# Performance work log

Measured on AMD Instinct MI355X. Metric: run time of the kernel, lower is better.

Reference implementation:

```python
import jax, jax.numpy as jnp
import numpy as np

B, K, N, D = 64, 16, 65536, 256


def setup_inputs() -> dict:
    key = jax.random.key(0)
    ks = jax.random.split(key, 7)
    slots = jax.random.normal(ks[0], (B, K, D), dtype=jnp.float32)
    attention_maps = jax.random.uniform(ks[1], (B, K, N), dtype=jnp.float32)
    semantic_confidence = jax.random.uniform(ks[2], (B, K), dtype=jnp.float32)
    # quality_net params: Linear(D, D//4) -> ReLU -> Dropout(eval: identity) -> Linear(D//4, 1) -> Sigmoid
    H = D // 4
    W1 = jax.random.normal(ks[3], (D, H), dtype=jnp.float32) / np.sqrt(D)
    b1 = jnp.zeros((H,), dtype=jnp.float32)
    W2 = jax.random.normal(ks[4], (H, 1), dtype=jnp.float32) / np.sqrt(H)
    b2 = jnp.zeros((1,), dtype=jnp.float32)
    return {"slots": slots, "attention_maps": attention_maps,
            "semantic_confidence": semantic_confidence,
            "W1": W1, "b1": b1, "W2": W2, "b2": b2}


def reference(slots, attention_maps, semantic_confidence, W1, b1, W2, b2):
    Bk, Kk, Nk = attention_maps.shape
    winners = jnp.argmax(attention_maps, axis=1)                      # [B, N]
    # one-hot winner mask [B, K, N] (replaces the Python K-loop in the source)
    mask = (winners[:, None, :] == jnp.arange(Kk)[None, :, None]).astype(attention_maps.dtype)
    winning_attn = jnp.sum(attention_maps * mask, axis=2)             # [B, K]
    total_attn = jnp.sum(attention_maps, axis=2)                      # [B, K]
    attn_quality = winning_attn / (total_attn + 1e-8)

    # learned quality: tiny MLP (dropout is identity at eval)
    h = jax.nn.relu(jnp.einsum('bkd,dh->bkh', slots, W1) + b1)
    learned_quality = jax.nn.sigmoid(jnp.einsum('bkh,ho->bko', h, W2) + b2)[..., 0]  # [B, K]

    w_attn, w_learned, w_conf = 0.4, 0.4, 0.2
    quality = w_attn * attn_quality + w_learned * learned_quality
    quality = quality * w_conf + semantic_confidence * (1.0 - w_conf)
    return quality
```

## Files before the change

### kernel.cpp

```cpp
#include <hip/hip_runtime.h>
#include <math.h>

#define B_ 64
#define K_ 16
#define N_ 65536
#define D_ 256
#define H_ 64

#define N4_ (N_ / 4)
#define CHUNKS_ 32
#define TPB_ 256
#define COLS_ (N4_ / CHUNKS_)
#define ITERS_ (COLS_ / TPB_)

typedef float f32x4 __attribute__((ext_vector_type(4)));


__global__ __launch_bounds__(TPB_) void attn_stats_kernel(const float* __restrict__ attn,
                                                          float* __restrict__ ws) {
    const int b = blockIdx.x / CHUNKS_;
    const int chunk = blockIdx.x % CHUNKS_;
    const f32x4* base = reinterpret_cast<const f32x4*>(attn) + (size_t)b * K_ * N4_;

    float tot[K_], win[K_];
#pragma unroll
    for (int k = 0; k < K_; ++k) { tot[k] = 0.0f; win[k] = 0.0f; }

#pragma unroll
    for (int it = 0; it < ITERS_; ++it) {
        const int c = chunk * COLS_ + it * TPB_ + threadIdx.x;
        f32x4 f = __builtin_nontemporal_load(&base[c]);
        float m0 = f.x, m1 = f.y, m2 = f.z, m3 = f.w;
        int i0 = 0, i1 = 0, i2 = 0, i3 = 0;
        tot[0] += (f.x + f.y) + (f.z + f.w);
#pragma unroll
        for (int k = 1; k < K_; ++k) {
            f = __builtin_nontemporal_load(&base[(size_t)k * N4_ + c]);
            tot[k] += (f.x + f.y) + (f.z + f.w);
            if (f.x > m0) { m0 = f.x; i0 = k; }
            if (f.y > m1) { m1 = f.y; i1 = k; }
            if (f.z > m2) { m2 = f.z; i2 = k; }
            if (f.w > m3) { m3 = f.w; i3 = k; }
        }
#pragma unroll
        for (int k = 0; k < K_; ++k) {
            win[k] += ((i0 == k) ? m0 : 0.0f) + ((i1 == k) ? m1 : 0.0f) +
                      ((i2 == k) ? m2 : 0.0f) + ((i3 == k) ? m3 : 0.0f);
        }
    }

#pragma unroll
    for (int k = 0; k < K_; ++k) {
        float t = tot[k], w = win[k];
#pragma unroll
        for (int s = 1; s < 64; s <<= 1) {
            t += __shfl_xor(t, s, 64);
            w += __shfl_xor(w, s, 64);
        }
        tot[k] = t; win[k] = w;
    }

    __shared__ float s_tot[4][K_];
    __shared__ float s_win[4][K_];
    const int lane = threadIdx.x & 63;
    const int wv = threadIdx.x >> 6;
    if (lane == 0) {
#pragma unroll
        for (int k = 0; k < K_; ++k) { s_tot[wv][k] = tot[k]; s_win[wv][k] = win[k]; }
    }
    __syncthreads();
    if (threadIdx.x < 2 * K_) {
        const int k = threadIdx.x & (K_ - 1);
        float v;
        if (threadIdx.x < K_) {
            v = (s_tot[0][k] + s_tot[1][k]) + (s_tot[2][k] + s_tot[3][k]);
        } else {
            v = (s_win[0][k] + s_win[1][k]) + (s_win[2][k] + s_win[3][k]);
        }
        ws[(size_t)blockIdx.x * (2 * K_) + threadIdx.x] = v;
    }
}

__global__ __launch_bounds__(64) void finalize_kernel(const float* __restrict__ slots,
                                                      const float* __restrict__ conf,
                                                      const float* __restrict__ W1,
                                                      const float* __restrict__ b1,
                                                      const float* __restrict__ W2,
                                                      const float* __restrict__ b2,
                                                      const float* __restrict__ ws,
                                                      float* __restrict__ out) {
    const int bk = blockIdx.x;
    const int b = bk / K_;
    const int k = bk % K_;
    const int j = threadIdx.x;

    __shared__ float s_slot[D_];
    reinterpret_cast<float4*>(s_slot)[j] =
        reinterpret_cast<const float4*>(slots + (size_t)bk * D_)[j];

    const int ch = j & 31;
    float red = (j < 32) ? ws[(size_t)(b * CHUNKS_ + ch) * (2 * K_) + k]
                         : ws[(size_t)(b * CHUNKS_ + ch) * (2 * K_) + K_ + k];
#pragma unroll
    for (int s = 1; s < 32; s <<= 1) red += __shfl_xor(red, s, 64);

    __syncthreads();

    float acc = b1[j];
#pragma unroll 8
    for (int d = 0; d < D_; ++d) {
        acc = fmaf(s_slot[d], W1[d * H_ + j], acc);
    }
    const float h = fmaxf(acc, 0.0f);
    float val = h * W2[j];
#pragma unroll
    for (int s = 1; s < 64; s <<= 1) val += __shfl_xor(val, s, 64);

    const float w = __shfl(red, 32, 64);
    if (j == 0) {
        const float t = red;
        const float lq = 1.0f / (1.0f + expf(-(val + b2[0])));
        const float aq = w / (t + 1e-8f);
        const float q = 0.4f * aq + 0.4f * lq;
        out[bk] = q * 0.2f + conf[bk] * 0.8f;
    }
}

extern "C" void kernel_launch(void* const* d_in, const int* in_sizes, int n_in,
                              void* d_out, int out_size, void* d_ws, size_t ws_size,
                              hipStream_t stream) {
    const float* slots = (const float*)d_in[0];
    const float* attn  = (const float*)d_in[1];
    const float* conf  = (const float*)d_in[2];
    const float* W1    = (const float*)d_in[3];
    const float* b1    = (const float*)d_in[4];
    const float* W2    = (const float*)d_in[5];
    const float* b2    = (const float*)d_in[6];
    float* out = (float*)d_out;
    float* ws  = (float*)d_ws;

    attn_stats_kernel<<<B_ * CHUNKS_, TPB_, 0, stream>>>(attn, ws);
    finalize_kernel<<<B_ * K_, 64, 0, stream>>>(slots, conf, W1, b1, W2, b2, ws, out);
}
```

Before: 60.96 us.

## Fuse quality MLP into attention stats kernel and use transpose-style wave reduction

Moves the per-slot MLP into the streaming attention-stats kernel. With B*CHUNKS equal to B*K there is one MLP per block, and it runs before or after streaming depending on block parity so its latency can hide behind memory traffic. Halves the chunk count, stops unrolling the outer loop, and replaces the 32 per-register butterfly reductions with a recursive-halving exchange that needs far fewer shuffles. It also writes per-wave partials so the block-level shared-memory reduction goes away. The finalize step becomes a light combine kernel, at the cost of fewer blocks (1024) and extra synchronization inside the streaming kernel.

```diff
diff --git a/kernel.cpp b/kernel.cpp
--- a/kernel.cpp
+++ b/kernel.cpp
@@ -8,27 +8,94 @@
 #define H_ 64
 
 #define N4_ (N_ / 4)
-#define CHUNKS_ 32
+#define CHUNKS_ 16
 #define TPB_ 256
 #define COLS_ (N4_ / CHUNKS_)
 #define ITERS_ (COLS_ / TPB_)
+#define NWAVE_ (TPB_ / 64)
+
+#define PART_FLOATS_ (B_ * CHUNKS_ * NWAVE_ * 32)
+#define LQ_OFF_ PART_FLOATS_
 
 typedef float f32x4 __attribute__((ext_vector_type(4)));
 
+__device__ __forceinline__ float reduce16_xchg(float v[16], int lane) {
+    int n = 16;
+#pragma unroll
+    for (int m = 1; m <= 8; m <<= 1) {
+        const bool keep_lo = ((lane & m) == 0);
+        n >>= 1;
+#pragma unroll
+        for (int j = 0; j < n; ++j) {
+            const float sent = keep_lo ? v[j + n] : v[j];
+            const float recv = __shfl_xor(sent, m, 64);
+            const float kept = keep_lo ? v[j] : v[j + n];
+            v[j] = kept + recv;
+        }
+    }
+    float r = v[0];
+    r += __shfl_xor(r, 16, 64);
+    r += __shfl_xor(r, 32, 64);
+    return r;
+}
+
+__device__ __forceinline__ void run_mlp(int bk, const float* __restrict__ slots,
+                                        const float* __restrict__ W1,
+                                        const float* __restrict__ b1,
+                                        const float* __restrict__ W2,
+                                        const float* __restrict__ b2,
+                                        float* __restrict__ ws,
+                                        float* s_slot, float* s_h) {
+    const int t = threadIdx.x;
+    const int j = t & 63;
+    const int q = t >> 6;
+    s_slot[t] = slots[(size_t)bk * D_ + t];
+    __syncthreads();
+    float p = 0.0f;
+#pragma unroll
+    for (int d = 0; d < 64; ++d) {
+        p = fmaf(s_slot[q * 64 + d], W1[(q * 64 + d) * H_ + j], p);
+    }
+    s_h[t] = p;
+    __syncthreads();
+    if (t < 64) {
+        float h = (s_h[t] + s_h[64 + t]) + (s_h[128 + t] + s_h[192 + t]) + b1[t];
+        h = fmaxf(h, 0.0f);
+        float val = h * W2[t];
+#pragma unroll
+        for (int s = 1; s < 64; s <<= 1) val += __shfl_xor(val, s, 64);
+        if (t == 0) ws[LQ_OFF_ + bk] = 1.0f / (1.0f + expf(-(val + b2[0])));
+    }
+    __syncthreads();
+}
 
 __global__ __launch_bounds__(TPB_) void attn_stats_kernel(const float* __restrict__ attn,
+                                                          const float* __restrict__ slots,
+                                                          const float* __restrict__ W1,
+                                                          const float* __restrict__ b1,
+                                                          const float* __restrict__ W2,
+                                                          const float* __restrict__ b2,
                                                           float* __restrict__ ws) {
-    const int b = blockIdx.x / CHUNKS_;
-    const int chunk = blockIdx.x % CHUNKS_;
-    const f32x4* base = reinterpret_cast<const f32x4*>(attn) + (size_t)b * K_ * N4_;
+    __shared__ float s_slot[D_];
+    __shared__ float s_h[TPB_];
+
+    const int bid = blockIdx.x;
+    const int b = bid / CHUNKS_;
+    const int chunk = bid % CHUNKS_;
+    const bool mlp_first = (bid & 1);
+
+    if (mlp_first) run_mlp(bid, slots, W1, b1, W2, b2, ws, s_slot, s_h);
+
+    const f32x4* base = reinterpret_cast<const f32x4*>(attn) +
+                        (size_t)b * K_ * N4_ + (size_t)chunk * COLS_;
 
     float tot[K_], win[K_];
 #pragma unroll
     for (int k = 0; k < K_; ++k) { tot[k] = 0.0f; win[k] = 0.0f; }
 
-#pragma unroll
+#pragma unroll 1
     for (int it = 0; it < ITERS_; ++it) {
-        const int c = chunk * COLS_ + it * TPB_ + threadIdx.x;
+        const int c = it * TPB_ + threadIdx.x;
         f32x4 f = __builtin_nontemporal_load(&base[c]);
         float m0 = f.x, m1 = f.y, m2 = f.z, m3 = f.w;
         int i0 = 0, i1 = 0, i2 = 0, i3 = 0;
@@ -49,81 +116,41 @@
         }
     }
 
-#pragma unroll
-    for (int k = 0; k < K_; ++k) {
-        float t = tot[k], w = win[k];
-#pragma unroll
-        for (int s = 1; s < 64; s <<= 1) {
-            t += __shfl_xor(t, s, 64);
-            w += __shfl_xor(w, s, 64);
-        }
-        tot[k] = t; win[k] = w;
-    }
+    if (!mlp_first) run_mlp(bid, slots, W1, b1, W2, b2, ws, s_slot, s_h);
 
-    __shared__ float s_tot[4][K_];
-    __shared__ float s_win[4][K_];
     const int lane = threadIdx.x & 63;
-    const int wv = threadIdx.x >> 6;
-    if (lane == 0) {
-#pragma unroll
-        for (int k = 0; k < K_; ++k) { s_tot[wv][k] = tot[k]; s_win[wv][k] = win[k]; }
-    }
-    __syncthreads();
-    if (threadIdx.x < 2 * K_) {
-        const int k = threadIdx.x & (K_ - 1);
-        float v;
-        if (threadIdx.x < K_) {
-            v = (s_tot[0][k] + s_tot[1][k]) + (s_tot[2][k] + s_tot[3][k]);
-        } else {
-            v = (s_win[0][k] + s_win[1][k]) + (s_win[2][k] + s_win[3][k]);
-        }
-        ws[(size_t)blockIdx.x * (2 * K_) + threadIdx.x] = v;
+    const float tr = reduce16_xchg(tot, lane);
+    const float wr = reduce16_xchg(win, lane);
+    if (lane < 16) {
+        const int k = ((lane & 1) << 3) | ((lane & 2) << 1) |
+                      ((lane & 4) >> 1) | ((lane & 8) >> 3);
+        const int wv = threadIdx.x >> 6;
+        float* dst = ws + ((size_t)bid * NWAVE_ + wv) * 32;
+        dst[k] = tr;
+        dst[16 + k] = wr;
     }
 }
 
-__global__ __launch_bounds__(64) void finalize_kernel(const float* __restrict__ slots,
-                                                      const float* __restrict__ conf,
-                                                      const float* __restrict__ W1,
-                                                      const float* __restrict__ b1,
-                                                      const float* __restrict__ W2,
-                                                      const float* __restrict__ b2,
-                                                      const float* __restrict__ ws,
-                                                      float* __restrict__ out) {
-    const int bk = blockIdx.x;
+__global__ __launch_bounds__(64) void combine_kernel(const float* __restrict__ conf,
+                                                     const float* __restrict__ ws,
+                                                     float* __restrict__ out) {
+    const int bk = blockIdx.x * 64 + threadIdx.x;
     const int b = bk / K_;
     const int k = bk % K_;
-    const int j = threadIdx.x;
-
-    __shared__ float s_slot[D_];
-    reinterpret_cast<float4*>(s_slot)[j] =
-        reinterpret_cast<const float4*>(slots + (size_t)bk * D_)[j];
-
-    const int ch = j & 31;
-    float red = (j < 32) ? ws[(size_t)(b * CHUNKS_ + ch) * (2 * K_) + k]
-                         : ws[(size_t)(b * CHUNKS_ + ch) * (2 * K_) + K_ + k];
+    float tot = 0.0f, win = 0.0f;
 #pragma unroll
-    for (int s = 1; s < 32; s <<= 1) red += __shfl_xor(red, s, 64);
-
-    __syncthreads();
-
-    float acc = b1[j];
-#pragma unroll 8
-    for (int d = 0; d < D_; ++d) {
-        acc = fmaf(s_slot[d], W1[d * H_ + j], acc);
+    for (int ch = 0; ch < CHUNKS_; ++ch) {
+#pragma unroll
+        for (int wv = 0; wv < NWAVE_; ++wv) {
+            const float* p = ws + ((size_t)(b * CHUNKS_ + ch) * NWAVE_ + wv) * 32;
+            tot += p[k];
+            win += p[16 + k];
+        }
     }
-    const float h = fmaxf(acc, 0.0f);
-    float val = h * W2[j];
-#pragma unroll
-    for (int s = 1; s < 64; s <<= 1) val += __shfl_xor(val, s, 64);
-
-    const float w = __shfl(red, 32, 64);
-    if (j == 0) {
-        const float t = red;
-        const float lq = 1.0f / (1.0f + expf(-(val + b2[0])));
-        const float aq = w / (t + 1e-8f);
-        const float q = 0.4f * aq + 0.4f * lq;
-        out[bk] = q * 0.2f + conf[bk] * 0.8f;
-    }
+    const float lq = ws[LQ_OFF_ + bk];
+    const float aq = win / (tot + 1e-8f);
+    const float q = 0.4f * aq + 0.4f * lq;
+    out[bk] = q * 0.2f + conf[bk] * 0.8f;
 }
 
 extern "C" void kernel_launch(void* const* d_in, const int* in_sizes, int n_in,
@@ -139,6 +166,6 @@
     float* out = (float*)d_out;
     float* ws  = (float*)d_ws;
 
-    attn_stats_kernel<<<B_ * CHUNKS_, TPB_, 0, stream>>>(attn, ws);
-    finalize_kernel<<<B_ * K_, 64, 0, stream>>>(slots, conf, W1, b1, W2, b2, ws, out);
+    attn_stats_kernel<<<B_ * CHUNKS_, TPB_, 0, stream>>>(attn, slots, W1, b1, W2, b2, ws);
+    combine_kernel<<<(B_ * K_) / 64, 64, 0, stream>>>(conf, ws, out);
 }
```

New measurement: 81.51 us. 33.7% more time.

## Fold quality MLP into attention-stats kernel and shrink finalize to tiny combine

Applied to the files above, without the earlier changes.

Moves the slot MLP computation into the first 64 blocks of the attention statistics kernel, where each wave computes four rows and shares each W1 load across them. The learned-quality values go to the workspace, and the second kernel becomes a small 4-block combine that sums chunk partials per thread. It also drops full unrolling of the outer streaming loop and folds the chunk offset into the base pointer. The aim is to cut the serialized tail of the 1024-block finalize kernel. The cost is extra work in a few stats blocks, which may lengthen the critical path.

```diff
diff --git a/kernel.cpp b/kernel.cpp
--- a/kernel.cpp
+++ b/kernel.cpp
@@ -13,22 +13,33 @@
 #define COLS_ (N4_ / CHUNKS_)
 #define ITERS_ (COLS_ / TPB_)
 
+#define MLP_BLOCKS_ 64
+#define ROWS_PER_BLK_ (B_ * K_ / MLP_BLOCKS_)
+
+#define PART_FLOATS_ (B_ * CHUNKS_ * 32)
+#define LQ_OFF_ PART_FLOATS_
+
 typedef float f32x4 __attribute__((ext_vector_type(4)));
 
-
 __global__ __launch_bounds__(TPB_) void attn_stats_kernel(const float* __restrict__ attn,
+                                                          const float* __restrict__ slots,
+                                                          const float* __restrict__ W1,
+                                                          const float* __restrict__ b1,
+                                                          const float* __restrict__ W2,
+                                                          const float* __restrict__ b2,
                                                           float* __restrict__ ws) {
-    const int b = blockIdx.x / CHUNKS_;
-    const int chunk = blockIdx.x % CHUNKS_;
-    const f32x4* base = reinterpret_cast<const f32x4*>(attn) + (size_t)b * K_ * N4_;
+    const int bid = blockIdx.x;
+    const int b = bid / CHUNKS_;
+    const int chunk = bid % CHUNKS_;
+    const f32x4* base = reinterpret_cast<const f32x4*>(attn) +
+                        (size_t)b * K_ * N4_ + (size_t)chunk * COLS_;
 
     float tot[K_], win[K_];
 #pragma unroll
     for (int k = 0; k < K_; ++k) { tot[k] = 0.0f; win[k] = 0.0f; }
 
-#pragma unroll
     for (int it = 0; it < ITERS_; ++it) {
-        const int c = chunk * COLS_ + it * TPB_ + threadIdx.x;
+        const int c = it * TPB_ + threadIdx.x;
         f32x4 f = __builtin_nontemporal_load(&base[c]);
         float m0 = f.x, m1 = f.y, m2 = f.z, m3 = f.w;
         int i0 = 0, i1 = 0, i2 = 0, i3 = 0;
@@ -77,53 +88,62 @@
         } else {
             v = (s_win[0][k] + s_win[1][k]) + (s_win[2][k] + s_win[3][k]);
         }
-        ws[(size_t)blockIdx.x * (2 * K_) + threadIdx.x] = v;
+        ws[(size_t)bid * (2 * K_) + threadIdx.x] = v;
+    }
+
+    if (bid < MLP_BLOCKS_) {
+        const int j = lane;
+        const int g = wv;
+        const int row0 = bid * ROWS_PER_BLK_ + g * 4;
+        float a0 = 0.0f, a1 = 0.0f, a2 = 0.0f, a3 = 0.0f;
+        const float* s0 = slots + (size_t)(row0 + 0) * D_;
+        const float* s1 = slots + (size_t)(row0 + 1) * D_;
+        const float* s2 = slots + (size_t)(row0 + 2) * D_;
+        const float* s3 = slots + (size_t)(row0 + 3) * D_;
+#pragma unroll 8
+        for (int d = 0; d < D_; ++d) {
+            const float w1v = W1[d * H_ + j];
+            a0 = fmaf(s0[d], w1v, a0);
+            a1 = fmaf(s1[d], w1v, a1);
+            a2 = fmaf(s2[d], w1v, a2);
+            a3 = fmaf(s3[d], w1v, a3);
+        }
+        const float b1v = b1[j], w2v = W2[j];
+        float v0 = fmaxf(a0 + b1v, 0.0f) * w2v;
+        float v1 = fmaxf(a1 + b1v, 0.0f) * w2v;
+        float v2 = fmaxf(a2 + b1v, 0.0f) * w2v;
+        float v3 = fmaxf(a3 + b1v, 0.0f) * w2v;
+#pragma unroll
+        for (int s = 1; s < 64; s <<= 1) {
+            v0 += __shfl_xor(v0, s, 64);
+            v1 += __shfl_xor(v1, s, 64);
+            v2 += __shfl_xor(v2, s, 64);
+            v3 += __shfl_xor(v3, s, 64);
+        }
+        if (lane < 4) {
+            const float val = (lane == 0) ? v0 : (lane == 1) ? v1 : (lane == 2) ? v2 : v3;
+            ws[LQ_OFF_ + row0 + lane] = 1.0f / (1.0f + expf(-(val + b2[0])));
+        }
     }
 }
 
-__global__ __launch_bounds__(64) void finalize_kernel(const float* __restrict__ slots,
-                                                      const float* __restrict__ conf,
-                                                      const float* __restrict__ W1,
-                                                      const float* __restrict__ b1,
-                                                      const float* __restrict__ W2,
-                                                      const float* __restrict__ b2,
+__global__ __launch_bounds__(256) void combine_kernel(const float* __restrict__ conf,
                                                       const float* __restrict__ ws,
                                                       float* __restrict__ out) {
-    const int bk = blockIdx.x;
+    const int bk = blockIdx.x * 256 + threadIdx.x;
     const int b = bk / K_;
     const int k = bk % K_;
-    const int j = threadIdx.x;
-
-    __shared__ float s_slot[D_];
-    reinterpret_cast<float4*>(s_slot)[j] =
-        reinterpret_cast<const float4*>(slots + (size_t)bk * D_)[j];
-
-    const int ch = j & 31;
-    float red = (j < 32) ? ws[(size_t)(b * CHUNKS_ + ch) * (2 * K_) + k]
-                         : ws[(size_t)(b * CHUNKS_ + ch) * (2 * K_) + K_ + k];
+    float tot = 0.0f, win = 0.0f;
 #pragma unroll
-    for (int s = 1; s < 32; s <<= 1) red += __shfl_xor(red, s, 64);
-
-    __syncthreads();
-
-    float acc = b1[j];
-#pragma unroll 8
-    for (int d = 0; d < D_; ++d) {
-        acc = fmaf(s_slot[d], W1[d * H_ + j], acc);
+    for (int ch = 0; ch < CHUNKS_; ++ch) {
+        const float* p = ws + (size_t)(b * CHUNKS_ + ch) * (2 * K_);
+        tot += p[k];
+        win += p[K_ + k];
     }
-    const float h = fmaxf(acc, 0.0f);
-    float val = h * W2[j];
-#pragma unroll
-    for (int s = 1; s < 64; s <<= 1) val += __shfl_xor(val, s, 64);
-
-    const float w = __shfl(red, 32, 64);
-    if (j == 0) {
-        const float t = red;
-        const float lq = 1.0f / (1.0f + expf(-(val + b2[0])));
-        const float aq = w / (t + 1e-8f);
-        const float q = 0.4f * aq + 0.4f * lq;
-        out[bk] = q * 0.2f + conf[bk] * 0.8f;
-    }
+    const float lq = ws[LQ_OFF_ + bk];
+    const float aq = win / (tot + 1e-8f);
+    const float q = 0.4f * aq + 0.4f * lq;
+    out[bk] = q * 0.2f + conf[bk] * 0.8f;
 }
 
 extern "C" void kernel_launch(void* const* d_in, const int* in_sizes, int n_in,
@@ -139,6 +159,6 @@
     float* out = (float*)d_out;
     float* ws  = (float*)d_ws;
 
-    attn_stats_kernel<<<B_ * CHUNKS_, TPB_, 0, stream>>>(attn, ws);
-    finalize_kernel<<<B_ * K_, 64, 0, stream>>>(slots, conf, W1, b1, W2, b2, ws, out);
+    attn_stats_kernel<<<B_ * CHUNKS_, TPB_, 0, stream>>>(attn, slots, W1, b1, W2, b2, ws);
+    combine_kernel<<<(B_ * K_) / 256, 256, 0, stream>>>(conf, ws, out);
 }
```

Measured after the change: 51.72 us. 1.18x faster.
